# Kernel tuning notes

Measured on AMD Instinct MI355X. Metric: run time of the kernel, lower is better.

The kernel has to match this reference:

```python
import jax, jax.numpy as jnp
from jax import lax
import numpy as np

B, H, W = 2, 48, 48
C_IN, C_OUT = 96, 192
D_INNER, N_STATE, DT_RANK, K = 192, 16, 6, 4  # VMamba: expand=2, d_state=16, dt_rank=ceil(C/16)
EPS = 1e-5


def setup_inputs() -> dict:
    ks = jax.random.split(jax.random.key(0), 16)
    s = 0.02
    r = lambda k, sh, sc=s: jax.random.normal(k, sh, jnp.float32) * sc
    d, N, R = D_INNER, N_STATE, DT_RANK
    return {
        "x": jax.random.normal(ks[0], (B, C_IN, H, W), jnp.float32),
        "ln_g": jnp.ones((C_IN,), jnp.float32),
        "ln_b": jnp.zeros((C_IN,), jnp.float32),
        "in_proj_w": r(ks[1], (2 * d, C_IN)),
        "dwconv_w": r(ks[2], (d, 1, 3, 3)),
        "dwconv_b": jnp.zeros((d,), jnp.float32),
        "x_proj_w": r(ks[3], (K, R + 2 * N, d)),
        "dt_w": r(ks[4], (K, d, R)),
        "dt_b": r(ks[5], (K, d), 0.1),
        "A_logs": jnp.tile(jnp.log(jnp.arange(1, N + 1, dtype=jnp.float32)), (K, d, 1)),
        "Ds": jnp.ones((K, d), jnp.float32),
        "out_norm_g": jnp.ones((d,), jnp.float32),
        "out_norm_b": jnp.zeros((d,), jnp.float32),
        "out_proj_w": r(ks[6], (C_IN, d)),
        "w1": r(ks[7], (C_OUT, C_IN, 1, 1)),
        "b1": jnp.zeros((C_OUT,), jnp.float32),
        "w31": r(ks[8], (C_OUT, C_IN, 3, 3)),
        "b31": jnp.zeros((C_OUT,), jnp.float32),
        "w32": r(ks[9], (C_OUT, C_IN, 3, 3)),
        "b32": jnp.zeros((C_OUT,), jnp.float32),
        "w33": r(ks[10], (C_OUT, C_OUT, 3, 3)),
        "b33": jnp.zeros((C_OUT,), jnp.float32),
        "bn_g": jnp.ones((3 * C_OUT,), jnp.float32),
        "bn_b": jnp.zeros((3 * C_OUT,), jnp.float32),
        "bn_m": r(ks[11], (3 * C_OUT,), 0.1),
        "bn_v": jax.random.uniform(ks[12], (3 * C_OUT,), jnp.float32) + 0.5,
        "prelu_a": jnp.float32(0.25),
    }


def _layernorm(x, g, b):
    m = jnp.mean(x, -1, keepdims=True)
    v = jnp.var(x, -1, keepdims=True)
    return (x - m) * lax.rsqrt(v + EPS) * g + b


def _conv(x, w, b, stride, pad, groups=1):
    y = lax.conv_general_dilated(x, w, (stride, stride), [(pad, pad), (pad, pad)],
                                 dimension_numbers=("NCHW", "OIHW", "NCHW"),
                                 feature_group_count=groups)
    return y + b[None, :, None, None]


def _ss2d(x, in_proj_w, dwconv_w, dwconv_b, x_proj_w, dt_w, dt_b, A_logs, Ds,
          out_norm_g, out_norm_b, out_proj_w):
    # x: (B, H, W, C)
    Bb, Hh, Ww, C = x.shape
    d, N, R = D_INNER, N_STATE, DT_RANK
    L = Hh * Ww
    xz = jnp.einsum("bhwc,ec->bhwe", x, in_proj_w)  # (B,H,W,2d)
    xin, z = jnp.split(xz, 2, axis=-1)
    xc = jnp.transpose(xin, (0, 3, 1, 2))           # (B,d,H,W)
    xc = jax.nn.silu(_conv(xc, dwconv_w, dwconv_b, 1, 1, groups=d))
    # 4 scan directions: row-major, col-major, and their reverses
    x_flat = xc.reshape(Bb, d, L)
    x_t = jnp.transpose(xc, (0, 1, 3, 2)).reshape(Bb, d, L)
    xs = jnp.stack([x_flat, x_t, x_flat[:, :, ::-1], x_t[:, :, ::-1]], axis=1)  # (B,K,d,L)
    x_dbl = jnp.einsum("bkdl,kcd->bkcl", xs, x_proj_w)
    dts, Bs, Cs = x_dbl[:, :, :R], x_dbl[:, :, R:R + N], x_dbl[:, :, R + N:]
    delta = jax.nn.softplus(jnp.einsum("bkrl,kdr->bkdl", dts, dt_w) + dt_b[None, :, :, None])
    A = -jnp.exp(A_logs)                                   # (K,d,N)
    dA = jnp.exp(jnp.einsum("bkdl,kdn->lbkdn", delta, A))  # (L,B,K,d,N)
    dBu = jnp.einsum("bkdl,bknl,bkdl->lbkdn", delta, Bs, xs)
    Cseq = jnp.transpose(Cs, (3, 0, 1, 2))                 # (L,B,K,N)

    def step(h, inp):
        dA_t, dBu_t, c_t = inp
        h = dA_t * h + dBu_t
        return h, jnp.einsum("bkdn,bkn->bkd", h, c_t)

    h0 = jnp.zeros((Bb, K, d, N), x.dtype)
    _, ys = lax.scan(step, h0, (dA, dBu, Cseq))            # ys: (L,B,K,d)
    ys = jnp.transpose(ys, (1, 2, 3, 0)) + xs * Ds[None, :, :, None]  # (B,K,d,L)

    def t_back(a):  # undo the HW transpose of col-major scans
        return jnp.transpose(a.reshape(Bb, d, Ww, Hh), (0, 1, 3, 2)).reshape(Bb, d, L)

    y = ys[:, 0] + ys[:, 2, :, ::-1] + t_back(ys[:, 1]) + t_back(ys[:, 3, :, ::-1])
    y = _layernorm(jnp.transpose(y, (0, 2, 1)), out_norm_g, out_norm_b).reshape(Bb, Hh, Ww, d)
    y = y * jax.nn.silu(z)
    return jnp.einsum("bhwd,cd->bhwc", y, out_proj_w)


def reference(x, ln_g, ln_b, in_proj_w, dwconv_w, dwconv_b, x_proj_w, dt_w, dt_b,
              A_logs, Ds, out_norm_g, out_norm_b, out_proj_w,
              w1, b1, w31, b31, w32, b32, w33, b33,
              bn_g, bn_b, bn_m, bn_v, prelu_a):
    # VSSBlock: residual + SS2D on LayerNorm'd NHWC features
    x_nhwc = jnp.transpose(x, (0, 2, 3, 1))
    x_nhwc = x_nhwc + _ss2d(_layernorm(x_nhwc, ln_g, ln_b), in_proj_w, dwconv_w,
                            dwconv_b, x_proj_w, dt_w, dt_b, A_logs, Ds,
                            out_norm_g, out_norm_b, out_proj_w)
    xm = jnp.transpose(x_nhwc, (0, 3, 1, 2))  # (B,C,H,W)
    # multi-branch stride-2 downsample
    x1 = _conv(xm, w1, b1, 2, 0)
    x2 = _conv(xm, w31, b31, 2, 1)
    x3 = _conv(_conv(xm, w32, b32, 2, 1), w33, b33, 1, 1)
    out = jnp.concatenate([x1, x2, x3], axis=1)  # (B, 3*C_OUT, H/2, W/2)
    # BatchNorm2d (inference, running stats) + PReLU(single param)
    out = (out - bn_m[None, :, None, None]) * lax.rsqrt(bn_v + EPS)[None, :, None, None] \
          * bn_g[None, :, None, None] + bn_b[None, :, None, None]
    return jnp.where(out > 0, out, prelu_a * out)
```

## Files before the change

kernel.cpp:

```cpp
#include <hip/hip_runtime.h>
#include <math.h>

#define BB_ 2
#define HH 48
#define WW 48
#define LL 2304
#define CIN 96
#define DD 192
#define KK 4
#define NN 16
#define RR 6
#define NCH 96
#define LC 24
#define COUT 192
#define OH 24
#define OW 24
#define OHW 576
#define NPX 1152
#define NTOT 4608
#define EPSF 1e-5f

typedef __attribute__((ext_vector_type(8))) short bf16x8;
typedef __attribute__((ext_vector_type(4))) float f32x4;

__device__ __forceinline__ short f2bf(float f) {
  unsigned u = __float_as_uint(f);
  unsigned r = (u + 0x7fffu + ((u >> 16) & 1u)) >> 16;
  return (short)r;
}

__global__ __launch_bounds__(256) void k_prep(const float* __restrict__ x,
                                              const float* __restrict__ g,
                                              const float* __restrict__ b,
                                              const float* __restrict__ inw,
                                              const float* __restrict__ xpw,
                                              const float* __restrict__ w31,
                                              const float* __restrict__ w32,
                                              const float* __restrict__ w33,
                                              const float* __restrict__ w1,
                                              const float* __restrict__ wout,
                                              float* __restrict__ stats,
                                              float* __restrict__ WgT,
                                              float* __restrict__ sWg,
                                              float* __restrict__ sWb,
                                              float* __restrict__ At3,
                                              short* __restrict__ At1b,
                                              short* __restrict__ At2b,
                                              short* __restrict__ woutb) {
  int bx = blockIdx.x;
  int tid = threadIdx.x;
  if (bx < 72) {
    int bb = bx / 36; int l0 = (bx % 36) * 64;
    int p = tid >> 2, q = tid & 3;
    int l = l0 + p;
    const float* xp = x + bb * CIN * LL + l;
    float s = 0.f, ss = 0.f;
    for (int c = q; c < CIN; c += 4) { float v = xp[c * LL]; s += v; ss += v * v; }
    s += __shfl_xor(s, 1, 64); s += __shfl_xor(s, 2, 64);
    ss += __shfl_xor(ss, 1, 64); ss += __shfl_xor(ss, 2, 64);
    if (q == 0) {
      float m = s / CIN; float var = ss / CIN - m * m;
      stats[(bb * LL + l) * 2 + 0] = m;
      stats[(bb * LL + l) * 2 + 1] = rsqrtf(var + EPSF);
    }
  } else if (bx == 72) {
    for (int e = tid; e < 2 * DD; e += 256) {
      float swg = 0.f, swb = 0.f;
      for (int c = 0; c < CIN; c++) {
        float w = inw[e * CIN + c];
        float wg = w * g[c];
        WgT[c * 384 + e] = wg;
        swg += wg; swb += w * b[c];
      }
      sWg[e] = swg; sWb[e] = swb;
    }
  } else if (bx < 217) {
    int idx = (bx - 73) * 256 + tid;
    if (idx < 192 * 192) {
      int m = idx % 192, d = idx / 192;
      At3[idx] = (m < 152) ? xpw[m * 192 + d] : 0.f;
    }
  } else if (bx < 2161) {
    int i = (bx - 217) * 256 + tid;
    if (i < 497664) {
      float v;
      if (i < 165888) v = w31[i];
      else if (i < 331776) v = w32[i - 165888];
      else {
        int k = i % 864; int m = i / 864 - 384;
        v = (k % 9 == 4) ? w1[m * 96 + k / 9] : 0.f;
      }
      At1b[i] = f2bf(v);
    }
  } else if (bx < 3457) {
    int i = (bx - 2161) * 256 + tid;
    if (i < 331776) At2b[i] = f2bf(w33[i]);
  } else {
    int i = (bx - 3457) * 256 + tid;
    if (i < 18432) woutb[i] = f2bf(wout[i]);
  }
}

__global__ __launch_bounds__(256) void k_dwconv(const float* __restrict__ xin,
                                                const float* __restrict__ wdw,
                                                const float* __restrict__ bdw,
                                                float* __restrict__ xs,
                                                float* __restrict__ xsl) {
  __shared__ float vt[32 * 50];
  int bid = blockIdx.x;
  int bb = bid / 288; int r = bid % 288; int dg = r / 72; int tile = r % 72;
  int l0 = tile * 32;
  int d0 = dg * 48;
  for (int i = threadIdx.x; i < 32 * 48; i += 256) {
    int lj = i & 31, dl = i >> 5;
    int d = d0 + dl;
    int l = l0 + lj;
    int h = l / WW, w = l % WW;
    const float* xp = xin + (bb * DD + d) * LL;
    const float* wq = wdw + d * 9;
    float acc = bdw[d];
#pragma unroll
    for (int kh = 0; kh < 3; kh++) {
      int ih = h + kh - 1; if (ih < 0 || ih >= HH) continue;
#pragma unroll
      for (int kw = 0; kw < 3; kw++) {
        int iw = w + kw - 1; if (iw < 0 || iw >= WW) continue;
        acc += xp[ih * WW + iw] * wq[kh * 3 + kw];
      }
    }
    float v = acc / (1.f + __expf(-acc));
    vt[lj * 50 + dl] = v;
    xsl[(size_t)d * NTOT + bb * LL + l] = v;
  }
  __syncthreads();
  for (int j = threadIdx.x; j < 32 * 48; j += 256) {
    int lj = j / 48, dl = j - lj * 48;
    int d = d0 + dl;
    int l = l0 + lj;
    int h = l / WW, w = l % WW;
    int lt = w * HH + h;
    float v = vt[lj * 50 + dl];
    xs[((size_t)(bb * 2 + 0) * LL + l) * DD + d] = v;
    xs[((size_t)(bb * 2 + 1) * LL + lt) * DD + d] = v;
  }
}

__global__ __launch_bounds__(256) void k_dtsplit(const float* __restrict__ C1,
                                                 const float* __restrict__ dtw,
                                                 const float* __restrict__ dtb,
                                                 float* __restrict__ Bsb,
                                                 float* __restrict__ Csb,
                                                 float* __restrict__ delta) {
  __shared__ float lds[38 * 33];
  int bid = blockIdx.x;
  int tile = bid % 72; int bk = bid / 72; int bb = bk >> 2; int k = bk & 3;
  int l0 = tile * 32;
  int tid = threadIdx.x;
  for (int i = tid; i < 38 * 32; i += 256) {
    int r = i >> 5, lj = i & 31;
    lds[r * 33 + lj] = C1[(size_t)(k * 38 + r) * NTOT + bb * LL + l0 + lj];
  }
  __syncthreads();
  for (int i = tid; i < 32 * 16; i += 256) {
    int lj = i >> 4, n = i & 15;
    int l = l0 + lj; int h = l / WW, w = l % WW; int lt = w * HH + h;
    int pos = (k == 0) ? l : (k == 1) ? lt : (k == 2) ? (LL - 1 - l) : (LL - 1 - lt);
    size_t base = ((size_t)bk * LL + pos) * NN + n;
    Bsb[base] = lds[(6 + n) * 33 + lj];
    Csb[base] = lds[(22 + n) * 33 + lj];
  }
  for (int i = tid; i < 32 * 192; i += 256) {
    int lj = i / 192, d = i - lj * 192;
    int l = l0 + lj; int h = l / WW, w = l % WW; int lt = w * HH + h;
    int pos = (k == 0) ? l : (k == 1) ? lt : (k == 2) ? (LL - 1 - l) : (LL - 1 - lt);
    const float* wd = dtw + (k * DD + d) * RR;
    float acc = dtb[k * DD + d];
#pragma unroll
    for (int r = 0; r < RR; r++) acc += wd[r] * lds[r * 33 + lj];
    float sp = acc > 20.f ? acc : log1pf(__expf(acc));
    delta[((size_t)bk * LL + pos) * DD + d] = sp;
  }
}

__global__ __launch_bounds__(192) void k_scan1(const float* __restrict__ delta,
                                               const float* __restrict__ xs,
                                               const float* __restrict__ Bsb,
                                               const float* __restrict__ A_logs,
                                               float* __restrict__ Pbuf,
                                               float* __restrict__ Sbuf) {
  __shared__ float Bls[LC * NN];
  int bid = blockIdx.x;
  int c = bid % NCH; int bk = bid / NCH; int k = bk & 3; int bb = bk >> 2;
  int t0 = c * LC;
  int d = threadIdx.x;
  const float* bp = Bsb + ((size_t)bk * LL + t0) * NN;
  for (int i = d; i < LC * NN; i += 192) Bls[i] = bp[i];
  float A[NN];
  {
    const float4* ap = (const float4*)(A_logs + (k * DD + d) * NN);
#pragma unroll
    for (int j = 0; j < 4; j++) {
      float4 a4 = ap[j];
      A[4 * j + 0] = -__expf(a4.x); A[4 * j + 1] = -__expf(a4.y);
      A[4 * j + 2] = -__expf(a4.z); A[4 * j + 3] = -__expf(a4.w);
    }
  }
  bool seq = true;
#pragma unroll
  for (int n = 0; n < NN; n++) seq = seq && (fabsf(A[n] + (float)(n + 1)) < 1e-3f);
  float h[NN];
#pragma unroll
  for (int n = 0; n < NN; n++) h[n] = 0.f;
  float sd = 0.f;
  __syncthreads();
  const float* dp = delta + ((size_t)bk * LL + t0) * DD + d;
  const float* xpb = xs + ((size_t)(bb * 2 + (k & 1)) * LL) * DD + d;
  const float* xp; int xstep;
  if (k < 2) { xp = xpb + (size_t)t0 * DD; xstep = DD; }
  else       { xp = xpb + (size_t)(LL - 1 - t0) * DD; xstep = -DD; }
#pragma unroll 2
  for (int t = 0; t < LC; ++t) {
    float dt = dp[t * DD];
    float xv = xp[t * xstep];
    float u = dt * xv;
    sd += dt;
    float dA[NN];
    if (seq) {
      float q = __expf(-dt);
      float q2 = q * q, q4 = q2 * q2, q8 = q4 * q4;
      dA[0] = q; dA[1] = q2; dA[2] = q2 * q; dA[3] = q4;
      dA[4] = q4 * q; dA[5] = q4 * q2; dA[6] = q4 * dA[2]; dA[7] = q8;
      dA[8] = q8 * q; dA[9] = q8 * q2; dA[10] = q8 * dA[2]; dA[11] = q8 * q4;
      dA[12] = q8 * dA[4]; dA[13] = q8 * dA[5]; dA[14] = q8 * dA[6]; dA[15] = q8 * q8;
    } else {
#pragma unroll
      for (int n = 0; n < NN; n++) dA[n] = __expf(dt * A[n]);
    }
    const float4* b4 = (const float4*)&Bls[t * NN];
#pragma unroll
    for (int j = 0; j < 4; j++) {
      float4 bv = b4[j];
      h[4 * j + 0] = dA[4 * j + 0] * h[4 * j + 0] + u * bv.x;
      h[4 * j + 1] = dA[4 * j + 1] * h[4 * j + 1] + u * bv.y;
      h[4 * j + 2] = dA[4 * j + 2] * h[4 * j + 2] + u * bv.z;
      h[4 * j + 3] = dA[4 * j + 3] * h[4 * j + 3] + u * bv.w;
    }
  }
  int chn = (bk * DD + d) * NN;
  float* pp = Pbuf + (size_t)c * 24576 + chn;
  float* sp = Sbuf + (size_t)c * 24576 + chn;
#pragma unroll
  for (int n = 0; n < NN; n++) { pp[n] = __expf(A[n] * sd); sp[n] = h[n]; }
}

__global__ __launch_bounds__(256) void k_scan2(const float* __restrict__ Pbuf,
                                               const float* __restrict__ Sbuf,
                                               float* __restrict__ Hinit) {
  int idx = blockIdx.x * 256 + threadIdx.x;
  float h = 0.f;
  for (int c = 0; c < NCH; c++) {
    Hinit[(size_t)c * 24576 + idx] = h;
    h = Pbuf[(size_t)c * 24576 + idx] * h + Sbuf[(size_t)c * 24576 + idx];
  }
}

__global__ __launch_bounds__(192) void k_scan3(const float* __restrict__ delta,
                                               const float* __restrict__ xs,
                                               const float* __restrict__ Bsb,
                                               const float* __restrict__ Csb,
                                               const float* __restrict__ A_logs,
                                               const float* __restrict__ Ds,
                                               const float* __restrict__ Hinit,
                                               float* __restrict__ ys) {
  __shared__ float Bls[LC * NN];
  __shared__ float Cls[LC * NN];
  int bid = blockIdx.x;
  int c = bid % NCH; int bk = bid / NCH; int k = bk & 3; int bb = bk >> 2;
  int t0 = c * LC;
  int d = threadIdx.x;
  const float* bp = Bsb + ((size_t)bk * LL + t0) * NN;
  const float* cp = Csb + ((size_t)bk * LL + t0) * NN;
  for (int i = d; i < LC * NN; i += 192) { Bls[i] = bp[i]; Cls[i] = cp[i]; }
  float A[NN];
  {
    const float4* ap = (const float4*)(A_logs + (k * DD + d) * NN);
#pragma unroll
    for (int j = 0; j < 4; j++) {
      float4 a4 = ap[j];
      A[4 * j + 0] = -__expf(a4.x); A[4 * j + 1] = -__expf(a4.y);
      A[4 * j + 2] = -__expf(a4.z); A[4 * j + 3] = -__expf(a4.w);
    }
  }
  bool seq = true;
#pragma unroll
  for (int n = 0; n < NN; n++) seq = seq && (fabsf(A[n] + (float)(n + 1)) < 1e-3f);
  float Dv = Ds[k * DD + d];
  float h[NN];
  {
    const float4* hp = (const float4*)(Hinit + (size_t)c * 24576 + (bk * DD + d) * NN);
#pragma unroll
    for (int j = 0; j < 4; j++) {
      float4 h4 = hp[j];
      h[4 * j + 0] = h4.x; h[4 * j + 1] = h4.y;
      h[4 * j + 2] = h4.z; h[4 * j + 3] = h4.w;
    }
  }
  __syncthreads();
  const float* dp = delta + ((size_t)bk * LL + t0) * DD + d;
  const float* xpb = xs + ((size_t)(bb * 2 + (k & 1)) * LL) * DD + d;
  const float* xp; int xstep;
  if (k < 2) { xp = xpb + (size_t)t0 * DD; xstep = DD; }
  else       { xp = xpb + (size_t)(LL - 1 - t0) * DD; xstep = -DD; }
  float* yp = ys + ((size_t)bk * LL + t0) * DD + d;
#pragma unroll 2
  for (int t = 0; t < LC; ++t) {
    float dt = dp[t * DD];
    float xv = xp[t * xstep];
    float u = dt * xv;
    float y = 0.f;
    float dA[NN];
    if (seq) {
      float q = __expf(-dt);
      float q2 = q * q, q4 = q2 * q2, q8 = q4 * q4;
      dA[0] = q; dA[1] = q2; dA[2] = q2 * q; dA[3] = q4;
      dA[4] = q4 * q; dA[5] = q4 * q2; dA[6] = q4 * dA[2]; dA[7] = q8;
      dA[8] = q8 * q; dA[9] = q8 * q2; dA[10] = q8 * dA[2]; dA[11] = q8 * q4;
      dA[12] = q8 * dA[4]; dA[13] = q8 * dA[5]; dA[14] = q8 * dA[6]; dA[15] = q8 * q8;
    } else {
#pragma unroll
      for (int n = 0; n < NN; n++) dA[n] = __expf(dt * A[n]);
    }
    const float4* b4 = (const float4*)&Bls[t * NN];
    const float4* c4 = (const float4*)&Cls[t * NN];
#pragma unroll
    for (int j = 0; j < 4; j++) {
      float4 bv = b4[j];
      float4 cc = c4[j];
      h[4 * j + 0] = dA[4 * j + 0] * h[4 * j + 0] + u * bv.x;
      h[4 * j + 1] = dA[4 * j + 1] * h[4 * j + 1] + u * bv.y;
      h[4 * j + 2] = dA[4 * j + 2] * h[4 * j + 2] + u * bv.z;
      h[4 * j + 3] = dA[4 * j + 3] * h[4 * j + 3] + u * bv.w;
      y += h[4 * j + 0] * cc.x + h[4 * j + 1] * cc.y
         + h[4 * j + 2] * cc.z + h[4 * j + 3] * cc.w;
    }
    yp[t * DD] = y + Dv * xv;
  }
}

__global__ __launch_bounds__(256) void k_combineF(const float* __restrict__ ys,
                                                  const float* __restrict__ z,
                                                  const float* __restrict__ ong,
                                                  const float* __restrict__ onb,
                                                  const short* __restrict__ Wbf,
                                                  const float* __restrict__ x,
                                                  float* __restrict__ xm) {
  __shared__ float yt[32 * 194];
  __shared__ unsigned Wlu[96 * 98];
  int bx = blockIdx.x; int bb = bx / 72; int l0 = (bx % 72) * 32;
  int tid = threadIdx.x;
  const unsigned* Wu = (const unsigned*)Wbf;
  for (int i = tid; i < 96 * 96; i += 256) {
    int e = i / 96, d2 = i - e * 96;
    Wlu[e * 98 + d2] = Wu[i];
  }
  for (int i = tid; i < 32 * DD; i += 256) {
    int p = i / DD, d = i - p * DD;
    int l = l0 + p; int h = l / WW, w = l - h * WW;
    int t1 = w * HH + h;
    float v = ys[(((size_t)bb * KK + 0) * LL + l) * DD + d]
            + ys[(((size_t)bb * KK + 1) * LL + t1) * DD + d]
            + ys[(((size_t)bb * KK + 2) * LL + (LL - 1 - l)) * DD + d]
            + ys[(((size_t)bb * KK + 3) * LL + (LL - 1 - t1)) * DD + d];
    yt[p * 194 + d] = v;
  }
  __syncthreads();
  int p = tid >> 3, q = tid & 7;
  int l = l0 + p;
  float s = 0.f, ss = 0.f;
  for (int d = q * 24; d < q * 24 + 24; d++) { float v = yt[p * 194 + d]; s += v; ss += v * v; }
  s += __shfl_xor(s, 1, 64); s += __shfl_xor(s, 2, 64); s += __shfl_xor(s, 4, 64);
  ss += __shfl_xor(ss, 1, 64); ss += __shfl_xor(ss, 2, 64); ss += __shfl_xor(ss, 4, 64);
  float m = s / DD, var = ss / DD - m * m;
  float rr = rsqrtf(var + EPSF);
  const float* zp = z + (bb * LL + l) * DD;
  for (int d = q * 24; d < q * 24 + 24; d++) {
    float v = (yt[p * 194 + d] - m) * rr * ong[d] + onb[d];
    float zv = zp[d];
    yt[p * 194 + d] = v * zv / (1.f + __expf(-zv));
  }
  __syncthreads();
  float acc[12];
#pragma unroll
  for (int j = 0; j < 12; j++) acc[j] = 0.f;
  for (int d2 = 0; d2 < 96; d2++) {
    float2 y2 = *(float2*)&yt[p * 194 + 2 * d2];
#pragma unroll
    for (int j = 0; j < 12; j++) {
      unsigned wv = Wlu[(q * 12 + j) * 98 + d2];
      float wlo = __uint_as_float(wv << 16);
      float whi = __uint_as_float(wv & 0xffff0000u);
      acc[j] += y2.x * wlo + y2.y * whi;
    }
  }
#pragma unroll
  for (int j = 0; j < 12; j++) {
    int e = q * 12 + j;
    size_t off = ((size_t)bb * CIN + e) * LL + l;
    xm[off] = x[off] + acc[j];
  }
}

template<int MT, int KCHUNK, int NB>
__global__ __launch_bounds__(256) void k_gemm(const float* __restrict__ At,
                                              const float* __restrict__ Bm,
                                              float* __restrict__ Cout) {
  __shared__ float As[16][64];
  __shared__ float Bs[16][64];
  int n0 = blockIdx.x * 64;
  int m0 = blockIdx.y * 64;
  int kz = blockIdx.z;
  int k0 = kz * KCHUNK;
  int tid = threadIdx.x;
  int lr = tid >> 4;
  int lc = (tid & 15) * 4;
  int tm = tid >> 4;
  int tn = tid & 15;
  float acc[4][4] = {};
  for (int ks = 0; ks < KCHUNK; ks += 16) {
    int kg = k0 + ks + lr;
    *(float4*)&As[lr][lc] = *(const float4*)&At[kg * MT + m0 + lc];
    *(float4*)&Bs[lr][lc] = *(const float4*)&Bm[(size_t)kg * NB + n0 + lc];
    __syncthreads();
#pragma unroll
    for (int kk = 0; kk < 16; kk++) {
      float4 a = *(float4*)&As[kk][tm * 4];
      float4 b = *(float4*)&Bs[kk][tn * 4];
      acc[0][0] += a.x * b.x; acc[0][1] += a.x * b.y; acc[0][2] += a.x * b.z; acc[0][3] += a.x * b.w;
      acc[1][0] += a.y * b.x; acc[1][1] += a.y * b.y; acc[1][2] += a.y * b.z; acc[1][3] += a.y * b.w;
      acc[2][0] += a.z * b.x; acc[2][1] += a.z * b.y; acc[2][2] += a.z * b.z; acc[2][3] += a.z * b.w;
      acc[3][0] += a.w * b.x; acc[3][1] += a.w * b.y; acc[3][2] += a.w * b.z; acc[3][3] += a.w * b.w;
    }
    __syncthreads();
  }
  float* cp = Cout + ((size_t)kz * MT + m0) * NB + n0;
#pragma unroll
  for (int i = 0; i < 4; i++) {
    float4 v = {acc[i][0], acc[i][1], acc[i][2], acc[i][3]};
    *(float4*)&cp[(size_t)(tm * 4 + i) * NB + tn * 4] = v;
  }
}

template<int MT, int KTOT, int KCHUNK, int CI, int IH, int STRIDE>
__global__ __launch_bounds__(256) void k_cgemm_mfma(const short* __restrict__ Abf,
                                                    const float* __restrict__ SRC,
                                                    float* __restrict__ Cout) {
  __shared__ short As[64][40];
  __shared__ short Bs[64][40];
  int n0 = blockIdx.x * 64;
  int m0 = blockIdx.y * 64;
  int kz = blockIdx.z;
  int k0 = kz * KCHUNK;
  int tid = threadIdx.x;
  int lane = tid & 63;
  int wv = tid >> 6;
  int row16 = lane & 15;
  int kg = lane >> 4;
  int sm = tid >> 2;
  int sk8 = (tid & 3) * 8;
  int n = n0 + sm;
  int bb = n / OHW; int rem = n - bb * OHW;
  int oh = rem / OW, ow = rem - oh * OW;
  f32x4 acc[4];
#pragma unroll
  for (int i = 0; i < 4; i++) acc[i] = (f32x4){0.f, 0.f, 0.f, 0.f};
  for (int ks = 0; ks < KCHUNK; ks += 32) {
    *(bf16x8*)&As[sm][sk8] =
        *(const bf16x8*)&Abf[(size_t)(m0 + sm) * KTOT + k0 + ks + sk8];
    bf16x8 bvv;
#pragma unroll
    for (int j = 0; j < 8; j++) {
      int k = k0 + ks + sk8 + j;
      int ci = k / 9; int r9 = k - ci * 9;
      int kh = r9 / 3, kw = r9 - kh * 3;
      int ih = STRIDE * oh + kh - 1;
      int iw = STRIDE * ow + kw - 1;
      float v = (ih >= 0 && ih < IH && iw >= 0 && iw < IH)
              ? SRC[((size_t)(bb * CI + ci) * IH + ih) * IH + iw] : 0.f;
      bvv[j] = f2bf(v);
    }
    *(bf16x8*)&Bs[sm][sk8] = bvv;
    __syncthreads();
    bf16x8 a = *(const bf16x8*)&As[wv * 16 + row16][kg * 8];
#pragma unroll
    for (int tn = 0; tn < 4; tn++) {
      bf16x8 b = *(const bf16x8*)&Bs[tn * 16 + row16][kg * 8];
      acc[tn] = __builtin_amdgcn_mfma_f32_16x16x32_bf16(a, b, acc[tn], 0, 0, 0);
    }
    __syncthreads();
  }
#pragma unroll
  for (int tn = 0; tn < 4; tn++) {
    int col = n0 + tn * 16 + row16;
    int rowb = m0 + wv * 16 + kg * 4;
#pragma unroll
    for (int i = 0; i < 4; i++)
      Cout[((size_t)kz * MT + rowb + i) * NPX + col] = acc[tn][i];
  }
}

template<int MT, int KD>
__global__ __launch_bounds__(256) void k_gemmF(const float* __restrict__ At,
                                               const float* __restrict__ Bm,
                                               int ldb, int boffB,
                                               float* __restrict__ C0,
                                               int ldc, int boffC,
                                               const float* __restrict__ a0,
                                               const float* __restrict__ a1,
                                               const float* __restrict__ a2,
                                               float* __restrict__ a3) {
  __shared__ float As[16][64];
  __shared__ float Bs[16][64];
  int n0 = blockIdx.x * 64;
  int m0 = blockIdx.y * 64;
  int bb = blockIdx.z;
  const float* B = Bm + (size_t)bb * boffB;
  int tid = threadIdx.x;
  int lr = tid >> 4;
  int lc = (tid & 15) * 4;
  int tm = tid >> 4;
  int tn = tid & 15;
  float acc[4][4] = {};
  for (int ks = 0; ks < KD; ks += 16) {
    *(float4*)&As[lr][lc] = *(const float4*)&At[(ks + lr) * MT + m0 + lc];
    *(float4*)&Bs[lr][lc] = *(const float4*)&B[(size_t)(ks + lr) * ldb + n0 + lc];
    __syncthreads();
#pragma unroll
    for (int kk = 0; kk < 16; kk++) {
      float4 a = *(float4*)&As[kk][tm * 4];
      float4 b = *(float4*)&Bs[kk][tn * 4];
      acc[0][0] += a.x * b.x; acc[0][1] += a.x * b.y; acc[0][2] += a.x * b.z; acc[0][3] += a.x * b.w;
      acc[1][0] += a.y * b.x; acc[1][1] += a.y * b.y; acc[1][2] += a.y * b.z; acc[1][3] += a.y * b.w;
      acc[2][0] += a.z * b.x; acc[2][1] += a.z * b.y; acc[2][2] += a.z * b.z; acc[2][3] += a.z * b.w;
      acc[3][0] += a.w * b.x; acc[3][1] += a.w * b.y; acc[3][2] += a.w * b.z; acc[3][3] += a.w * b.w;
    }
    __syncthreads();
  }
  int n = n0 + tn * 4;
  float m_[4], r_[4];
#pragma unroll
  for (int j = 0; j < 4; j++) {
    m_[j] = a0[((size_t)bb * LL + n + j) * 2];
    r_[j] = a0[((size_t)bb * LL + n + j) * 2 + 1];
  }
#pragma unroll
  for (int i = 0; i < 4; i++) {
    int e = m0 + tm * 4 + i;
    float swg = a1[e], swb = a2[e];
    float v0 = r_[0] * (acc[i][0] - m_[0] * swg) + swb;
    float v1 = r_[1] * (acc[i][1] - m_[1] * swg) + swb;
    float v2 = r_[2] * (acc[i][2] - m_[2] * swg) + swb;
    float v3 = r_[3] * (acc[i][3] - m_[3] * swg) + swb;
    if (e < DD) {
      float4 v = {v0, v1, v2, v3};
      *(float4*)&C0[(size_t)bb * boffC + (size_t)e * ldc + n] = v;
    } else {
      a3[((size_t)bb * LL + n + 0) * DD + (e - DD)] = v0;
      a3[((size_t)bb * LL + n + 1) * DD + (e - DD)] = v1;
      a3[((size_t)bb * LL + n + 2) * DD + (e - DD)] = v2;
      a3[((size_t)bb * LL + n + 3) * DD + (e - DD)] = v3;
    }
  }
}

__global__ __launch_bounds__(256) void k_reduce1(const float* __restrict__ Cp1,
                                                 const float* __restrict__ b1,
                                                 const float* __restrict__ b31,
                                                 const float* __restrict__ b32,
                                                 const float* __restrict__ bn_g,
                                                 const float* __restrict__ bn_b,
                                                 const float* __restrict__ bn_m,
                                                 const float* __restrict__ bn_v,
                                                 const float* __restrict__ prelu_a,
                                                 float* __restrict__ out,
                                                 float* __restrict__ t3) {
  int idx = blockIdx.x * 256 + threadIdx.x;
  if (idx >= 576 * NPX) return;
  int m = idx / NPX, n = idx % NPX;
  float s = 0.f;
#pragma unroll
  for (int c = 0; c < 9; c++) s += Cp1[(size_t)c * 576 * NPX + idx];
  int bb = n / OHW, o = n % OHW;
  if (m < 192) {
    s += b31[m];
    int cc = 192 + m;
    float scale = rsqrtf(bn_v[cc] + EPSF) * bn_g[cc];
    float v = s * scale + (bn_b[cc] - bn_m[cc] * scale);
    float a = prelu_a[0];
    out[((size_t)bb * 576 + cc) * OHW + o] = v > 0.f ? v : a * v;
  } else if (m < 384) {
    s += b32[m - 192];
    t3[((size_t)bb * COUT + (m - 192)) * OHW + o] = s;
  } else {
    s += b1[m - 384];
    int cc = m - 384;
    float scale = rsqrtf(bn_v[cc] + EPSF) * bn_g[cc];
    float v = s * scale + (bn_b[cc] - bn_m[cc] * scale);
    float a = prelu_a[0];
    out[((size_t)bb * 576 + cc) * OHW + o] = v > 0.f ? v : a * v;
  }
}

__global__ __launch_bounds__(256) void k_reduce2(const float* __restrict__ Cp2,
                                                 const float* __restrict__ b33,
                                                 const float* __restrict__ bn_g,
                                                 const float* __restrict__ bn_b,
                                                 const float* __restrict__ bn_m,
                                                 const float* __restrict__ bn_v,
                                                 const float* __restrict__ prelu_a,
                                                 float* __restrict__ out) {
  int idx = blockIdx.x * 256 + threadIdx.x;
  if (idx >= 192 * NPX) return;
  int m = idx / NPX, n = idx % NPX;
  float s = b33[m];
#pragma unroll
  for (int c = 0; c < 9; c++) s += Cp2[(size_t)c * 192 * NPX + idx];
  int bb = n / OHW, o = n % OHW;
  int cc = 384 + m;
  float scale = rsqrtf(bn_v[cc] + EPSF) * bn_g[cc];
  float v = s * scale + (bn_b[cc] - bn_m[cc] * scale);
  float a = prelu_a[0];
  out[((size_t)bb * 576 + cc) * OHW + o] = v > 0.f ? v : a * v;
}

extern "C" void kernel_launch(void* const* d_in, const int* in_sizes, int n_in,
                              void* d_out, int out_size, void* d_ws, size_t ws_size,
                              hipStream_t stream) {
  const float* x        = (const float*)d_in[0];
  const float* ln_g     = (const float*)d_in[1];
  const float* ln_b     = (const float*)d_in[2];
  const float* in_proj_w= (const float*)d_in[3];
  const float* dwconv_w = (const float*)d_in[4];
  const float* dwconv_b = (const float*)d_in[5];
  const float* x_proj_w = (const float*)d_in[6];
  const float* dt_w     = (const float*)d_in[7];
  const float* dt_b     = (const float*)d_in[8];
  const float* A_logs   = (const float*)d_in[9];
  const float* Ds       = (const float*)d_in[10];
  const float* out_norm_g = (const float*)d_in[11];
  const float* out_norm_b = (const float*)d_in[12];
  const float* out_proj_w = (const float*)d_in[13];
  const float* w1  = (const float*)d_in[14];
  const float* b1  = (const float*)d_in[15];
  const float* w31 = (const float*)d_in[16];
  const float* b31 = (const float*)d_in[17];
  const float* w32 = (const float*)d_in[18];
  const float* b32 = (const float*)d_in[19];
  const float* w33 = (const float*)d_in[20];
  const float* b33 = (const float*)d_in[21];
  const float* bn_g = (const float*)d_in[22];
  const float* bn_b = (const float*)d_in[23];
  const float* bn_m = (const float*)d_in[24];
  const float* bn_v = (const float*)d_in[25];
  const float* prelu_a = (const float*)d_in[26];

  float* ws = (float*)d_ws;
  float* stats = ws + 0;
  float* WgT   = ws + 16384;
  float* sWg   = ws + 65536;
  float* sWb   = ws + 66048;
  float* At3   = ws + 98304;
  short* At1b  = (short*)(ws + 147456);
  short* At2b  = (short*)(ws + 397312);
  short* woutb = (short*)(ws + 565248);
  float* xin   = ws + 2097152;
  float* z     = ws + 3145728;
  float* xs    = ws + 4194304;
  float* xsl   = ws + 8388608;
  float* C1    = ws + 9437184;
  float* delta = ws + 10485760;
  float* Bsb   = ws + 14155776;
  float* Csb   = ws + 14680064;
  float* Pbuf  = ws + 15728640;
  float* Sbuf  = ws + 18874368;
  float* Hinit = ws + 22020096;
  float* ys    = ws + 25165824;
  float* xm    = ws + 29360128;
  float* t3    = ws + 30408704;
  float* Cp1   = ws + 31457280;
  float* Cp2   = ws + 37748736;
  float* out = (float*)d_out;

  k_prep<<<3529, 256, 0, stream>>>(x, ln_g, ln_b, in_proj_w, x_proj_w,
                                   w31, w32, w33, w1, out_proj_w,
                                   stats, WgT, sWg, sWb, At3, At1b, At2b, woutb);
  k_gemmF<384, 96><<<dim3(36, 6, 2), 256, 0, stream>>>(
      WgT, x, LL, CIN * LL, xin, LL, DD * LL, stats, sWg, sWb, z);
  k_dwconv<<<576, 256, 0, stream>>>(xin, dwconv_w, dwconv_b, xs, xsl);
  k_gemm<192, 192, NTOT><<<dim3(72, 3, 1), 256, 0, stream>>>(At3, xsl, C1);
  k_dtsplit<<<576, 256, 0, stream>>>(C1, dt_w, dt_b, Bsb, Csb, delta);
  k_scan1<<<768, 192, 0, stream>>>(delta, xs, Bsb, A_logs, Pbuf, Sbuf);
  k_scan2<<<96, 256, 0, stream>>>(Pbuf, Sbuf, Hinit);
  k_scan3<<<768, 192, 0, stream>>>(delta, xs, Bsb, Csb, A_logs, Ds, Hinit, ys);
  k_combineF<<<144, 256, 0, stream>>>(ys, z, out_norm_g, out_norm_b, woutb, x, xm);
  k_cgemm_mfma<576, 864, 96, CIN, HH, 2><<<dim3(18, 9, 9), 256, 0, stream>>>(
      At1b, xm, Cp1);
  k_reduce1<<<2592, 256, 0, stream>>>(Cp1, b1, b31, b32, bn_g, bn_b, bn_m, bn_v,
                                      prelu_a, out, t3);
  k_cgemm_mfma<192, 1728, 192, COUT, OH, 1><<<dim3(18, 3, 9), 256, 0, stream>>>(
      At2b, t3, Cp2);
  k_reduce2<<<864, 256, 0, stream>>>(Cp2, b33, bn_g, bn_b, bn_m, bn_v, prelu_a, out);
}
```

Baseline: 186.8 us.

## Fuse x_proj GEMM with dt/B/C split using bf16 MFMA; shrink conv split-K

Replaces the fp32 x_proj GEMM and the separate dt-split kernel with one MFMA kernel. It reads bf16 activations in pixel-major layout and bf16 weights, keeps the projection tile in LDS, and writes B, C and softplus delta directly. It also cuts the split-K factor of both convolution GEMMs from 9 to 3 and 6, so the reduce kernels read fewer partial sums. The cost is bf16 rounding in the x_proj GEMM, and the larger K chunks per block leave fewer blocks in flight.

```diff
diff --git a/kernel.cpp b/kernel.cpp
--- a/kernel.cpp
+++ b/kernel.cpp
@@ -43,7 +43,7 @@
                                               float* __restrict__ WgT,
                                               float* __restrict__ sWg,
                                               float* __restrict__ sWb,
-                                              float* __restrict__ At3,
+                                              short* __restrict__ At3b,
                                               short* __restrict__ At1b,
                                               short* __restrict__ At2b,
                                               short* __restrict__ woutb) {
@@ -77,8 +77,8 @@
   } else if (bx < 217) {
     int idx = (bx - 73) * 256 + tid;
     if (idx < 192 * 192) {
-      int m = idx % 192, d = idx / 192;
-      At3[idx] = (m < 152) ? xpw[m * 192 + d] : 0.f;
+      int m = idx / 192;
+      At3b[idx] = (m < 152) ? f2bf(xpw[idx]) : (short)0;
     }
   } else if (bx < 2161) {
     int i = (bx - 217) * 256 + tid;
@@ -105,7 +105,7 @@
                                                 const float* __restrict__ wdw,
                                                 const float* __restrict__ bdw,
                                                 float* __restrict__ xs,
-                                                float* __restrict__ xsl) {
+                                                short* __restrict__ xsb) {
   __shared__ float vt[32 * 50];
   int bid = blockIdx.x;
   int bb = bid / 288; int r = bid % 288; int dg = r / 72; int tile = r % 72;
@@ -130,7 +130,6 @@
     }
     float v = acc / (1.f + __expf(-acc));
     vt[lj * 50 + dl] = v;
-    xsl[(size_t)d * NTOT + bb * LL + l] = v;
   }
   __syncthreads();
   for (int j = threadIdx.x; j < 32 * 48; j += 256) {
@@ -142,43 +141,90 @@
     float v = vt[lj * 50 + dl];
     xs[((size_t)(bb * 2 + 0) * LL + l) * DD + d] = v;
     xs[((size_t)(bb * 2 + 1) * LL + lt) * DD + d] = v;
-  }
-}
-
-__global__ __launch_bounds__(256) void k_dtsplit(const float* __restrict__ C1,
-                                                 const float* __restrict__ dtw,
-                                                 const float* __restrict__ dtb,
-                                                 float* __restrict__ Bsb,
-                                                 float* __restrict__ Csb,
-                                                 float* __restrict__ delta) {
-  __shared__ float lds[38 * 33];
-  int bid = blockIdx.x;
-  int tile = bid % 72; int bk = bid / 72; int bb = bk >> 2; int k = bk & 3;
-  int l0 = tile * 32;
+    xsb[((size_t)bb * LL + l) * DD + d] = f2bf(v);
+  }
+}
+
+__global__ __launch_bounds__(256) void k_xprojF(const short* __restrict__ At3b,
+                                                const short* __restrict__ xsb,
+                                                const float* __restrict__ dtw,
+                                                const float* __restrict__ dtb,
+                                                float* __restrict__ Bsb,
+                                                float* __restrict__ Csb,
+                                                float* __restrict__ delta) {
+  __shared__ short As[192][40];
+  __shared__ short Bs[32][40];
+  __shared__ float ct[152][33];
+  int p0 = blockIdx.x * 32;
   int tid = threadIdx.x;
-  for (int i = tid; i < 38 * 32; i += 256) {
-    int r = i >> 5, lj = i & 31;
-    lds[r * 33 + lj] = C1[(size_t)(k * 38 + r) * NTOT + bb * LL + l0 + lj];
+  int lane = tid & 63;
+  int wv = tid >> 6;
+  int row16 = lane & 15;
+  int kg = lane >> 4;
+  f32x4 acc[3][2];
+#pragma unroll
+  for (int j = 0; j < 3; j++)
+#pragma unroll
+    for (int nf = 0; nf < 2; nf++) acc[j][nf] = (f32x4){0.f, 0.f, 0.f, 0.f};
+  for (int ks = 0; ks < 192; ks += 32) {
+#pragma unroll
+    for (int it = 0; it < 3; it++) {
+      int slot = tid + 256 * it;
+      int sm = slot >> 2, sk8 = (slot & 3) * 8;
+      *(bf16x8*)&As[sm][sk8] = *(const bf16x8*)&At3b[(size_t)sm * 192 + ks + sk8];
+    }
+    if (tid < 128) {
+      int sn = tid >> 2, sk8 = (tid & 3) * 8;
+      *(bf16x8*)&Bs[sn][sk8] = *(const bf16x8*)&xsb[(size_t)(p0 + sn) * 192 + ks + sk8];
+    }
+    __syncthreads();
+#pragma unroll
+    for (int j = 0; j < 3; j++) {
+      bf16x8 a = *(const bf16x8*)&As[(wv * 3 + j) * 16 + row16][kg * 8];
+#pragma unroll
+      for (int nf = 0; nf < 2; nf++) {
+        bf16x8 b = *(const bf16x8*)&Bs[nf * 16 + row16][kg * 8];
+        acc[j][nf] = __builtin_amdgcn_mfma_f32_16x16x32_bf16(a, b, acc[j][nf], 0, 0, 0);
+      }
+    }
+    __syncthreads();
+  }
+#pragma unroll
+  for (int j = 0; j < 3; j++) {
+    int rowb = (wv * 3 + j) * 16 + kg * 4;
+#pragma unroll
+    for (int nf = 0; nf < 2; nf++) {
+      int col = nf * 16 + row16;
+#pragma unroll
+      for (int i = 0; i < 4; i++) {
+        int r = rowb + i;
+        if (r < 152) ct[r][col] = acc[j][nf][i];
+      }
+    }
   }
   __syncthreads();
-  for (int i = tid; i < 32 * 16; i += 256) {
-    int lj = i >> 4, n = i & 15;
-    int l = l0 + lj; int h = l / WW, w = l % WW; int lt = w * HH + h;
+  int bb = p0 / LL;
+  int lbase = p0 - bb * LL;
+  for (int i = tid; i < 2048; i += 256) {
+    int k = i >> 9; int rem = i & 511; int lj = rem >> 4; int n = rem & 15;
+    int l = lbase + lj; int h = l / WW, w = l - h * WW; int lt = w * HH + h;
     int pos = (k == 0) ? l : (k == 1) ? lt : (k == 2) ? (LL - 1 - l) : (LL - 1 - lt);
-    size_t base = ((size_t)bk * LL + pos) * NN + n;
-    Bsb[base] = lds[(6 + n) * 33 + lj];
-    Csb[base] = lds[(22 + n) * 33 + lj];
-  }
-  for (int i = tid; i < 32 * 192; i += 256) {
-    int lj = i / 192, d = i - lj * 192;
-    int l = l0 + lj; int h = l / WW, w = l % WW; int lt = w * HH + h;
-    int pos = (k == 0) ? l : (k == 1) ? lt : (k == 2) ? (LL - 1 - l) : (LL - 1 - lt);
-    const float* wd = dtw + (k * DD + d) * RR;
-    float acc = dtb[k * DD + d];
-#pragma unroll
-    for (int r = 0; r < RR; r++) acc += wd[r] * lds[r * 33 + lj];
-    float sp = acc > 20.f ? acc : log1pf(__expf(acc));
-    delta[((size_t)bk * LL + pos) * DD + d] = sp;
+    size_t base = ((size_t)(bb * 4 + k) * LL + pos) * NN + n;
+    Bsb[base] = ct[k * 38 + 6 + n][lj];
+    Csb[base] = ct[k * 38 + 22 + n][lj];
+  }
+  for (int k = 0; k < 4; k++) {
+    for (int i = tid; i < 32 * 192; i += 256) {
+      int lj = i / 192, d = i - lj * 192;
+      int l = lbase + lj; int h = l / WW, w = l - h * WW; int lt = w * HH + h;
+      int pos = (k == 0) ? l : (k == 1) ? lt : (k == 2) ? (LL - 1 - l) : (LL - 1 - lt);
+      const float* wd = dtw + (k * DD + d) * RR;
+      float a2 = dtb[k * DD + d];
+#pragma unroll
+      for (int r = 0; r < RR; r++) a2 += wd[r] * ct[k * 38 + r][lj];
+      float sp = a2 > 20.f ? a2 : log1pf(__expf(a2));
+      delta[((size_t)(bb * 4 + k) * LL + pos) * DD + d] = sp;
+    }
   }
 }
 
@@ -407,46 +453,6 @@
     int e = q * 12 + j;
     size_t off = ((size_t)bb * CIN + e) * LL + l;
     xm[off] = x[off] + acc[j];
-  }
-}
-
-template<int MT, int KCHUNK, int NB>
-__global__ __launch_bounds__(256) void k_gemm(const float* __restrict__ At,
-                                              const float* __restrict__ Bm,
-                                              float* __restrict__ Cout) {
-  __shared__ float As[16][64];
-  __shared__ float Bs[16][64];
-  int n0 = blockIdx.x * 64;
-  int m0 = blockIdx.y * 64;
-  int kz = blockIdx.z;
-  int k0 = kz * KCHUNK;
-  int tid = threadIdx.x;
-  int lr = tid >> 4;
-  int lc = (tid & 15) * 4;
-  int tm = tid >> 4;
-  int tn = tid & 15;
-  float acc[4][4] = {};
-  for (int ks = 0; ks < KCHUNK; ks += 16) {
-    int kg = k0 + ks + lr;
-    *(float4*)&As[lr][lc] = *(const float4*)&At[kg * MT + m0 + lc];
-    *(float4*)&Bs[lr][lc] = *(const float4*)&Bm[(size_t)kg * NB + n0 + lc];
-    __syncthreads();
-#pragma unroll
-    for (int kk = 0; kk < 16; kk++) {
-      float4 a = *(float4*)&As[kk][tm * 4];
-      float4 b = *(float4*)&Bs[kk][tn * 4];
-      acc[0][0] += a.x * b.x; acc[0][1] += a.x * b.y; acc[0][2] += a.x * b.z; acc[0][3] += a.x * b.w;
-      acc[1][0] += a.y * b.x; acc[1][1] += a.y * b.y; acc[1][2] += a.y * b.z; acc[1][3] += a.y * b.w;
-      acc[2][0] += a.z * b.x; acc[2][1] += a.z * b.y; acc[2][2] += a.z * b.z; acc[2][3] += a.z * b.w;
-      acc[3][0] += a.w * b.x; acc[3][1] += a.w * b.y; acc[3][2] += a.w * b.z; acc[3][3] += a.w * b.w;
-    }
-    __syncthreads();
-  }
-  float* cp = Cout + ((size_t)kz * MT + m0) * NB + n0;
-#pragma unroll
-  for (int i = 0; i < 4; i++) {
-    float4 v = {acc[i][0], acc[i][1], acc[i][2], acc[i][3]};
-    *(float4*)&cp[(size_t)(tm * 4 + i) * NB + tn * 4] = v;
   }
 }
 
@@ -588,7 +594,7 @@
   int m = idx / NPX, n = idx % NPX;
   float s = 0.f;
 #pragma unroll
-  for (int c = 0; c < 9; c++) s += Cp1[(size_t)c * 576 * NPX + idx];
+  for (int c = 0; c < 3; c++) s += Cp1[(size_t)c * 576 * NPX + idx];
   int bb = n / OHW, o = n % OHW;
   if (m < 192) {
     s += b31[m];
@@ -623,7 +629,7 @@
   int m = idx / NPX, n = idx % NPX;
   float s = b33[m];
 #pragma unroll
-  for (int c = 0; c < 9; c++) s += Cp2[(size_t)c * 192 * NPX + idx];
+  for (int c = 0; c < 6; c++) s += Cp2[(size_t)c * 192 * NPX + idx];
   int bb = n / OHW, o = n % OHW;
   int cc = 384 + m;
   float scale = rsqrtf(bn_v[cc] + EPSF) * bn_g[cc];
@@ -668,15 +674,14 @@
   float* WgT   = ws + 16384;
   float* sWg   = ws + 65536;
   float* sWb   = ws + 66048;
-  float* At3   = ws + 98304;
+  short* At3b  = (short*)(ws + 98304);
   short* At1b  = (short*)(ws + 147456);
   short* At2b  = (short*)(ws + 397312);
   short* woutb = (short*)(ws + 565248);
   float* xin   = ws + 2097152;
   float* z     = ws + 3145728;
   float* xs    = ws + 4194304;
-  float* xsl   = ws + 8388608;
-  float* C1    = ws + 9437184;
+  short* xsb   = (short*)(ws + 6291456);
   float* delta = ws + 10485760;
   float* Bsb   = ws + 14155776;
   float* Csb   = ws + 14680064;
@@ -687,26 +692,25 @@
   float* xm    = ws + 29360128;
   float* t3    = ws + 30408704;
   float* Cp1   = ws + 31457280;
-  float* Cp2   = ws + 37748736;
+  float* Cp2   = ws + 33554432;
   float* out = (float*)d_out;
 
   k_prep<<<3529, 256, 0, stream>>>(x, ln_g, ln_b, in_proj_w, x_proj_w,
                                    w31, w32, w33, w1, out_proj_w,
-                                   stats, WgT, sWg, sWb, At3, At1b, At2b, woutb);
+                                   stats, WgT, sWg, sWb, At3b, At1b, At2b, woutb);
   k_gemmF<384, 96><<<dim3(36, 6, 2), 256, 0, stream>>>(
       WgT, x, LL, CIN * LL, xin, LL, DD * LL, stats, sWg, sWb, z);
-  k_dwconv<<<576, 256, 0, stream>>>(xin, dwconv_w, dwconv_b, xs, xsl);
-  k_gemm<192, 192, NTOT><<<dim3(72, 3, 1), 256, 0, stream>>>(At3, xsl, C1);
-  k_dtsplit<<<576, 256, 0, stream>>>(C1, dt_w, dt_b, Bsb, Csb, delta);
+  k_dwconv<<<576, 256, 0, stream>>>(xin, dwconv_w, dwconv_b, xs, xsb);
+  k_xprojF<<<144, 256, 0, stream>>>(At3b, xsb, dt_w, dt_b, Bsb, Csb, delta);
   k_scan1<<<768, 192, 0, stream>>>(delta, xs, Bsb, A_logs, Pbuf, Sbuf);
   k_scan2<<<96, 256, 0, stream>>>(Pbuf, Sbuf, Hinit);
   k_scan3<<<768, 192, 0, stream>>>(delta, xs, Bsb, Csb, A_logs, Ds, Hinit, ys);
   k_combineF<<<144, 256, 0, stream>>>(ys, z, out_norm_g, out_norm_b, woutb, x, xm);
-  k_cgemm_mfma<576, 864, 96, CIN, HH, 2><<<dim3(18, 9, 9), 256, 0, stream>>>(
+  k_cgemm_mfma<576, 864, 288, CIN, HH, 2><<<dim3(18, 9, 3), 256, 0, stream>>>(
       At1b, xm, Cp1);
   k_reduce1<<<2592, 256, 0, stream>>>(Cp1, b1, b31, b32, bn_g, bn_b, bn_m, bn_v,
                                       prelu_a, out, t3);
-  k_cgemm_mfma<192, 1728, 192, COUT, OH, 1><<<dim3(18, 3, 9), 256, 0, stream>>>(
+  k_cgemm_mfma<192, 1728, 288, COUT, OH, 1><<<dim3(18, 3, 6), 256, 0, stream>>>(
       At2b, t3, Cp2);
   k_reduce2<<<864, 256, 0, stream>>>(Cp2, b33, bn_g, bn_b, bn_m, bn_v, prelu_a, out);
 }
```

New measurement: 206.1 us. 1.1x slower.
